# Optimization experiments

Measured on AMD Instinct MI355X. Metric: run time of the kernel, lower is better.

## Reference

```python
import jax, jax.numpy as jnp
import numpy as np

N_NODES = 50000
N_EDGES = 800000
IN_DIM = 128
HIDDEN = 128
OUT_DIM = 128


def setup_inputs() -> dict:
    key = jax.random.key(0)
    k1, k2, k3, k4, k5, k6 = jax.random.split(key, 6)
    X = jax.random.normal(k1, (N_NODES, IN_DIM), dtype=jnp.float32)
    W0 = jax.random.normal(k2, (HIDDEN, IN_DIM), dtype=jnp.float32) * (1.0 / np.sqrt(IN_DIM))
    W1 = jax.random.normal(k3, (OUT_DIM, HIDDEN), dtype=jnp.float32) * (1.0 / np.sqrt(HIDDEN))
    norm = jax.random.uniform(k4, (N_EDGES,), dtype=jnp.float32)
    src = jax.random.randint(k5, (N_EDGES,), 0, N_NODES, dtype=jnp.int32)
    dst = jax.random.randint(k6, (N_EDGES,), 0, N_NODES, dtype=jnp.int32)
    return {"X": X, "W0": W0, "W1": W1, "norm": norm, "src": src, "dst": dst}


def _propagate(S, src, dst, norm, n_nodes):
    # gather-scale-scatter: Z[dst] += S[src] * norm   (SpMM-style)
    msg = S[src] * norm[:, None]  # [E, d]
    return jax.ops.segment_sum(msg, dst, num_segments=n_nodes)


def reference(X, W0, W1, norm, src, dst):
    n = X.shape[0]
    # layer 1: linear (nn.Linear stores W as [out,in], so x @ W.T) + propagate + relu
    S0 = X @ W0.T                       # [N, hidden]
    H = jax.nn.relu(_propagate(S0, src, dst, norm, n))
    # dropout p=0.5 -> identity in eval mode (reference baseline)
    S1 = H @ W1.T                       # [N, out]
    Z = _propagate(S1, src, dst, norm, n)
    return (Z, H)
```

## Files before the change

### kernel.cpp

```cpp
#include <hip/hip_runtime.h>

#define DIM 128
#define NB 782
#define BCAP 1536

typedef __attribute__((ext_vector_type(8))) short bf16x8_t;
typedef __attribute__((ext_vector_type(4))) float f32x4_t;

__device__ __forceinline__ short f2bf(float f) {
    unsigned u = __float_as_uint(f);
    u += 0x7FFFu + ((u >> 16) & 1u);
    return (short)(u >> 16);
}
__device__ __forceinline__ float bf2f(short s) {
    return __uint_as_float(((unsigned)(unsigned short)s) << 16);
}

#define SC_VPT 16
__global__ __launch_bounds__(256) void bucket_scatter(const int* __restrict__ src,
                                                      const int* __restrict__ dst,
                                                      const float* __restrict__ norm,
                                                      int* __restrict__ bcursor,
                                                      int2* __restrict__ binned, int E) {
    __shared__ int hist[NB];
    __shared__ int base[NB];
    int t = threadIdx.x;
    for (int b = t; b < NB; b += 256) hist[b] = 0;
    __syncthreads();

    int e0 = blockIdx.x * (256 * SC_VPT);
    int bkts[SC_VPT];
    int pack[SC_VPT];
    int nrm[SC_VPT];
    #pragma unroll
    for (int k = 0; k < SC_VPT; k++) {
        int e = e0 + k * 256 + t;
        if (e < E) {
            int d = dst[e];
            bkts[k] = d >> 6;
            pack[k] = ((d & 63) << 26) | src[e];
            nrm[k]  = __float_as_int(norm[e]);
            atomicAdd(&hist[bkts[k]], 1);
        } else bkts[k] = -1;
    }
    __syncthreads();
    for (int b = t; b < NB; b += 256) {
        int c = hist[b];
        base[b] = b * BCAP + (c ? atomicAdd(&bcursor[b], c) : 0);
        hist[b] = 0;
    }
    __syncthreads();
    #pragma unroll
    for (int k = 0; k < SC_VPT; k++) {
        if (bkts[k] >= 0) {
            int pos = base[bkts[k]] + atomicAdd(&hist[bkts[k]], 1);
            binned[pos] = make_int2(pack[k], nrm[k]);
        }
    }
}


__global__ __launch_bounds__(256) void gemm_mfma(const float* __restrict__ A,
                                                 const float* __restrict__ W,
                                                 short* __restrict__ Cbf, int n,
                                                 int* __restrict__ bcursor_zero) {
    if (bcursor_zero != nullptr && blockIdx.x == 0) {
        for (int i = threadIdx.x; i < NB; i += 256) bcursor_zero[i] = 0;
    }

    int wave = threadIdx.x >> 6;
    int lane = threadIdx.x & 63;
    int l16  = lane & 15;
    int quad = lane >> 4;
    int r0 = blockIdx.x * 64 + wave * 16;

    int arow = r0 + l16;
    if (arow >= n) arow = n - 1;
    const float* Ar = A + (size_t)arow * DIM + quad * 8;

    bf16x8_t fa[4];
    #pragma unroll
    for (int kk = 0; kk < 4; kk++) {
        float4 x0 = *(const float4*)(Ar + kk * 32);
        float4 x1 = *(const float4*)(Ar + kk * 32 + 4);
        bf16x8_t f;
        f[0] = f2bf(x0.x); f[1] = f2bf(x0.y); f[2] = f2bf(x0.z); f[3] = f2bf(x0.w);
        f[4] = f2bf(x1.x); f[5] = f2bf(x1.y); f[6] = f2bf(x1.z); f[7] = f2bf(x1.w);
        fa[kk] = f;
    }

    #pragma unroll
    for (int ct = 0; ct < 8; ct++) {
        const float* Wr = W + (size_t)(ct * 16 + l16) * DIM + quad * 8;
        f32x4_t acc = {0.f, 0.f, 0.f, 0.f};
        #pragma unroll
        for (int kk = 0; kk < 4; kk++) {
            float4 w0 = *(const float4*)(Wr + kk * 32);
            float4 w1 = *(const float4*)(Wr + kk * 32 + 4);
            bf16x8_t fb;
            fb[0] = f2bf(w0.x); fb[1] = f2bf(w0.y); fb[2] = f2bf(w0.z); fb[3] = f2bf(w0.w);
            fb[4] = f2bf(w1.x); fb[5] = f2bf(w1.y); fb[6] = f2bf(w1.z); fb[7] = f2bf(w1.w);
            acc = __builtin_amdgcn_mfma_f32_16x16x32_bf16(fa[kk], fb, acc, 0, 0, 0);
        }
        #pragma unroll
        for (int j = 0; j < 4; j++) {
            int row = r0 + quad * 4 + j;
            if (row < n) Cbf[(size_t)row * DIM + ct * 16 + l16] = f2bf(acc[j]);
        }
    }
}


__global__ __launch_bounds__(512) void prop_bucket(const short* __restrict__ Sbf,
                                                   const int2* __restrict__ binned,
                                                   const int* __restrict__ bcnt,
                                                   float* __restrict__ out,
                                                   int n, int do_relu) {
    __shared__ int2 eds[BCAP];
    __shared__ int  hist[64];
    __shared__ int  offs_s[65];
    int b = blockIdx.x;
    int t = threadIdx.x;
    int cnt = bcnt[b];
    if (cnt > BCAP) cnt = BCAP;
    if (t < 64) hist[t] = 0;
    __syncthreads();

    const int2* eb = binned + (size_t)b * BCAP;
    for (int i = t; i < cnt; i += 512)
        atomicAdd(&hist[((unsigned)eb[i].x) >> 26], 1);
    __syncthreads();
    if (t < 64) {
        int v = hist[t];
        int s = v;
        #pragma unroll
        for (int o = 1; o < 64; o <<= 1) {
            int x = __shfl_up(s, o, 64);
            if (t >= o) s += x;
        }
        offs_s[t] = s - v;
        if (t == 63) offs_s[64] = s;
        hist[t] = s - v;
    }
    __syncthreads();
    for (int i = t; i < cnt; i += 512) {
        int2 e = eb[i];
        int pos = atomicAdd(&hist[((unsigned)e.x) >> 26], 1);
        eds[pos] = e;
    }
    __syncthreads();

    int wv   = t >> 6;
    int lane = t & 63;
    int q    = lane >> 4;
    int l16  = lane & 15;
    int node0 = b << 6;
    for (int nd = wv; nd < 64; nd += 8) {
        int beg = offs_s[nd];
        int end = offs_s[nd + 1];
        float acc[8] = {};
        int i = beg + q;
        for (; i + 4 < end; i += 8) {
            int2 e0 = eds[i];
            int2 e1 = eds[i + 4];
            bf16x8_t v0 = *(const bf16x8_t*)(Sbf + (size_t)((unsigned)e0.x & 0x3FFFFFF) * DIM + l16 * 8);
            bf16x8_t v1 = *(const bf16x8_t*)(Sbf + (size_t)((unsigned)e1.x & 0x3FFFFFF) * DIM + l16 * 8);
            float n0 = __int_as_float(e0.y);
            float n1 = __int_as_float(e1.y);
            #pragma unroll
            for (int j = 0; j < 8; j++) acc[j] += n0 * bf2f(v0[j]);
            #pragma unroll
            for (int j = 0; j < 8; j++) acc[j] += n1 * bf2f(v1[j]);
        }
        for (; i < end; i += 4) {
            int2 e = eds[i];
            bf16x8_t v = *(const bf16x8_t*)(Sbf + (size_t)((unsigned)e.x & 0x3FFFFFF) * DIM + l16 * 8);
            float nv = __int_as_float(e.y);
            #pragma unroll
            for (int j = 0; j < 8; j++) acc[j] += nv * bf2f(v[j]);
        }
        #pragma unroll
        for (int j = 0; j < 8; j++) {
            acc[j] += __shfl_xor(acc[j], 16, 64);
            acc[j] += __shfl_xor(acc[j], 32, 64);
        }
        int node = node0 + nd;
        if (q == 0 && node < n) {
            if (do_relu) {
                #pragma unroll
                for (int j = 0; j < 8; j++) acc[j] = fmaxf(acc[j], 0.f);
            }
            f32x4_t o0 = {acc[0], acc[1], acc[2], acc[3]};
            f32x4_t o1 = {acc[4], acc[5], acc[6], acc[7]};
            float* row = out + (size_t)node * DIM + l16 * 8;
            __builtin_nontemporal_store(o0, (f32x4_t*)row);
            __builtin_nontemporal_store(o1, (f32x4_t*)(row + 4));
        }
    }
}


extern "C" void kernel_launch(void* const* d_in, const int* in_sizes, int n_in,
                              void* d_out, int out_size, void* d_ws, size_t ws_size,
                              hipStream_t stream) {
    const float* X    = (const float*)d_in[0];
    const float* W0   = (const float*)d_in[1];
    const float* W1   = (const float*)d_in[2];
    const float* norm = (const float*)d_in[3];
    const int*   src  = (const int*)d_in[4];
    const int*   dst  = (const int*)d_in[5];

    const int N = in_sizes[0] / DIM;
    const int E = in_sizes[3];

    float* Z = (float*)d_out;
    float* H = (float*)d_out + (size_t)N * DIM;

    char* ws = (char*)d_ws;
    short* Sbf    = (short*)ws;
    size_t off    = (size_t)N * DIM * sizeof(short);
    int*   bcursor= (int*)(ws + off); off += (NB * 4 + 255) / 256 * 256;
    int2*  binned = (int2*)(ws + off); off += (size_t)NB * BCAP * 8;

    const int gemm_grid = (N + 63) / 64;

    gemm_mfma<<<gemm_grid, 256, 0, stream>>>(X, W0, Sbf, N, bcursor);
    bucket_scatter<<<(E + 256 * SC_VPT - 1) / (256 * SC_VPT), 256, 0, stream>>>(
        src, dst, norm, bcursor, binned, E);
    prop_bucket<<<NB, 512, 0, stream>>>(Sbf, binned, bcursor, H, N, 1);
    gemm_mfma<<<gemm_grid, 256, 0, stream>>>(H, W1, Sbf, N, nullptr);
    prop_bucket<<<NB, 512, 0, stream>>>(Sbf, binned, bcursor, Z, N, 0);
}
```

Before: 235.4 us.

## Fuse first GEMM with edge bucketing and reuse sorted edges in second propagate

Merges the first GEMM and the bucket-scatter kernel into a single launch, with blocks split by index, so the two independent phases can overlap. Zeroing of the bucket cursor moves to a hipMemsetAsync. The first propagate pass now writes its per-node sorted edge list and offsets to global memory. The second pass reads those back instead of re-histogramming and re-sorting in shared memory. This trades an extra global write and read of the edge list for removing the counting sort, and adds a memset launch.

```diff
diff --git a/kernel.cpp b/kernel.cpp
--- a/kernel.cpp
+++ b/kernel.cpp
@@ -3,6 +3,7 @@
 #define DIM 128
 #define NB 782
 #define BCAP 1536
+#define SC_VPT 16
 
 typedef __attribute__((ext_vector_type(8))) short bf16x8_t;
 typedef __attribute__((ext_vector_type(4))) float f32x4_t;
@@ -16,63 +17,14 @@
     return __uint_as_float(((unsigned)(unsigned short)s) << 16);
 }
 
-#define SC_VPT 16
-__global__ __launch_bounds__(256) void bucket_scatter(const int* __restrict__ src,
-                                                      const int* __restrict__ dst,
-                                                      const float* __restrict__ norm,
-                                                      int* __restrict__ bcursor,
-                                                      int2* __restrict__ binned, int E) {
-    __shared__ int hist[NB];
-    __shared__ int base[NB];
-    int t = threadIdx.x;
-    for (int b = t; b < NB; b += 256) hist[b] = 0;
-    __syncthreads();
-
-    int e0 = blockIdx.x * (256 * SC_VPT);
-    int bkts[SC_VPT];
-    int pack[SC_VPT];
-    int nrm[SC_VPT];
-    #pragma unroll
-    for (int k = 0; k < SC_VPT; k++) {
-        int e = e0 + k * 256 + t;
-        if (e < E) {
-            int d = dst[e];
-            bkts[k] = d >> 6;
-            pack[k] = ((d & 63) << 26) | src[e];
-            nrm[k]  = __float_as_int(norm[e]);
-            atomicAdd(&hist[bkts[k]], 1);
-        } else bkts[k] = -1;
-    }
-    __syncthreads();
-    for (int b = t; b < NB; b += 256) {
-        int c = hist[b];
-        base[b] = b * BCAP + (c ? atomicAdd(&bcursor[b], c) : 0);
-        hist[b] = 0;
-    }
-    __syncthreads();
-    #pragma unroll
-    for (int k = 0; k < SC_VPT; k++) {
-        if (bkts[k] >= 0) {
-            int pos = base[bkts[k]] + atomicAdd(&hist[bkts[k]], 1);
-            binned[pos] = make_int2(pack[k], nrm[k]);
-        }
-    }
-}
-
-
-__global__ __launch_bounds__(256) void gemm_mfma(const float* __restrict__ A,
-                                                 const float* __restrict__ W,
-                                                 short* __restrict__ Cbf, int n,
-                                                 int* __restrict__ bcursor_zero) {
-    if (bcursor_zero != nullptr && blockIdx.x == 0) {
-        for (int i = threadIdx.x; i < NB; i += 256) bcursor_zero[i] = 0;
-    }
-
+__device__ __forceinline__ void gemm_body(const float* __restrict__ A,
+                                          const float* __restrict__ W,
+                                          short* __restrict__ Cbf, int n, int blk) {
     int wave = threadIdx.x >> 6;
     int lane = threadIdx.x & 63;
     int l16  = lane & 15;
     int quad = lane >> 4;
-    int r0 = blockIdx.x * 64 + wave * 16;
+    int r0 = blk * 64 + wave * 16;
 
     int arow = r0 + l16;
     if (arow >= n) arow = n - 1;
@@ -110,74 +62,172 @@
     }
 }
 
+__device__ __forceinline__ void scatter_body(const int* __restrict__ src,
+                                             const int* __restrict__ dst,
+                                             const float* __restrict__ norm,
+                                             int* __restrict__ bcursor,
+                                             int2* __restrict__ binned, int E, int blk) {
+    __shared__ int hist[NB];
+    __shared__ int base[NB];
+    int t = threadIdx.x;
+    for (int b = t; b < NB; b += 256) hist[b] = 0;
+    __syncthreads();
+
+    int e0 = blk * (256 * SC_VPT);
+    int bkts[SC_VPT];
+    int pack[SC_VPT];
+    int nrm[SC_VPT];
+    #pragma unroll
+    for (int k = 0; k < SC_VPT; k++) {
+        int e = e0 + k * 256 + t;
+        if (e < E) {
+            int d = dst[e];
+            bkts[k] = d >> 6;
+            pack[k] = ((d & 63) << 26) | src[e];
+            nrm[k]  = __float_as_int(norm[e]);
+            atomicAdd(&hist[bkts[k]], 1);
+        } else bkts[k] = -1;
+    }
+    __syncthreads();
+    for (int b = t; b < NB; b += 256) {
+        int c = hist[b];
+        base[b] = b * BCAP + (c ? atomicAdd(&bcursor[b], c) : 0);
+        hist[b] = 0;
+    }
+    __syncthreads();
+    #pragma unroll
+    for (int k = 0; k < SC_VPT; k++) {
+        if (bkts[k] >= 0) {
+            int pos = base[bkts[k]] + atomicAdd(&hist[bkts[k]], 1);
+            binned[pos] = make_int2(pack[k], nrm[k]);
+        }
+    }
+}
+
+__global__ __launch_bounds__(256) void fused_gemm_scatter(
+        const float* __restrict__ X, const float* __restrict__ W0,
+        short* __restrict__ Sbf, int n,
+        const int* __restrict__ src, const int* __restrict__ dst,
+        const float* __restrict__ norm, int* __restrict__ bcursor,
+        int2* __restrict__ binned, int E, int gemmBlocks) {
+    if ((int)blockIdx.x < gemmBlocks)
+        gemm_body(X, W0, Sbf, n, blockIdx.x);
+    else
+        scatter_body(src, dst, norm, bcursor, binned, E, blockIdx.x - gemmBlocks);
+}
+
+__global__ __launch_bounds__(256) void gemm_mfma(const float* __restrict__ A,
+                                                 const float* __restrict__ W,
+                                                 short* __restrict__ Cbf, int n) {
+    gemm_body(A, W, Cbf, n, blockIdx.x);
+}
+
 
 __global__ __launch_bounds__(512) void prop_bucket(const short* __restrict__ Sbf,
                                                    const int2* __restrict__ binned,
                                                    const int* __restrict__ bcnt,
+                                                   int2* __restrict__ edges2,
+                                                   int* __restrict__ offs_g,
                                                    float* __restrict__ out,
-                                                   int n, int do_relu) {
+                                                   int n, int do_relu, int mode) {
+    __shared__ int2 raw[BCAP];
     __shared__ int2 eds[BCAP];
     __shared__ int  hist[64];
     __shared__ int  offs_s[65];
     int b = blockIdx.x;
     int t = threadIdx.x;
-    int cnt = bcnt[b];
-    if (cnt > BCAP) cnt = BCAP;
-    if (t < 64) hist[t] = 0;
-    __syncthreads();
-
-    const int2* eb = binned + (size_t)b * BCAP;
-    for (int i = t; i < cnt; i += 512)
-        atomicAdd(&hist[((unsigned)eb[i].x) >> 26], 1);
-    __syncthreads();
-    if (t < 64) {
-        int v = hist[t];
-        int s = v;
-        #pragma unroll
-        for (int o = 1; o < 64; o <<= 1) {
-            int x = __shfl_up(s, o, 64);
-            if (t >= o) s += x;
-        }
-        offs_s[t] = s - v;
-        if (t == 63) offs_s[64] = s;
-        hist[t] = s - v;
-    }
-    __syncthreads();
-    for (int i = t; i < cnt; i += 512) {
-        int2 e = eb[i];
-        int pos = atomicAdd(&hist[((unsigned)e.x) >> 26], 1);
-        eds[pos] = e;
-    }
-    __syncthreads();
+
+    if (mode == 0) {
+        int cnt = bcnt[b];
+        if (cnt > BCAP) cnt = BCAP;
+        if (t < 64) hist[t] = 0;
+        __syncthreads();
+        const int2* eb = binned + (size_t)b * BCAP;
+        for (int i = t; i < cnt; i += 512) {
+            int2 e = eb[i];
+            raw[i] = e;
+            atomicAdd(&hist[((unsigned)e.x) >> 26], 1);
+        }
+        __syncthreads();
+        if (t < 64) {
+            int v = hist[t];
+            int s = v;
+            #pragma unroll
+            for (int o = 1; o < 64; o <<= 1) {
+                int x = __shfl_up(s, o, 64);
+                if (t >= o) s += x;
+            }
+            offs_s[t] = s - v;
+            if (t == 63) offs_s[64] = s;
+            hist[t] = s - v;
+        }
+        __syncthreads();
+        for (int i = t; i < cnt; i += 512) {
+            int2 e = raw[i];
+            int pos = atomicAdd(&hist[((unsigned)e.x) >> 26], 1);
+            eds[pos] = e;
+        }
+        __syncthreads();
+        int2* e2 = edges2 + (size_t)b * BCAP;
+        for (int i = t; i < cnt; i += 512) e2[i] = eds[i];
+        if (t < 65) offs_g[b * 65 + t] = offs_s[t];
+    } else {
+        if (t < 65) offs_s[t] = offs_g[b * 65 + t];
+        __syncthreads();
+    }
 
     int wv   = t >> 6;
     int lane = t & 63;
     int q    = lane >> 4;
     int l16  = lane & 15;
     int node0 = b << 6;
+    const int2* eg = edges2 + (size_t)b * BCAP;
+
     for (int nd = wv; nd < 64; nd += 8) {
         int beg = offs_s[nd];
         int end = offs_s[nd + 1];
         float acc[8] = {};
         int i = beg + q;
-        for (; i + 4 < end; i += 8) {
-            int2 e0 = eds[i];
-            int2 e1 = eds[i + 4];
-            bf16x8_t v0 = *(const bf16x8_t*)(Sbf + (size_t)((unsigned)e0.x & 0x3FFFFFF) * DIM + l16 * 8);
-            bf16x8_t v1 = *(const bf16x8_t*)(Sbf + (size_t)((unsigned)e1.x & 0x3FFFFFF) * DIM + l16 * 8);
-            float n0 = __int_as_float(e0.y);
-            float n1 = __int_as_float(e1.y);
-            #pragma unroll
-            for (int j = 0; j < 8; j++) acc[j] += n0 * bf2f(v0[j]);
-            #pragma unroll
-            for (int j = 0; j < 8; j++) acc[j] += n1 * bf2f(v1[j]);
-        }
-        for (; i < end; i += 4) {
-            int2 e = eds[i];
-            bf16x8_t v = *(const bf16x8_t*)(Sbf + (size_t)((unsigned)e.x & 0x3FFFFFF) * DIM + l16 * 8);
-            float nv = __int_as_float(e.y);
-            #pragma unroll
-            for (int j = 0; j < 8; j++) acc[j] += nv * bf2f(v[j]);
+        if (mode == 0) {
+            for (; i + 4 < end; i += 8) {
+                int2 e0 = eds[i];
+                int2 e1 = eds[i + 4];
+                bf16x8_t v0 = *(const bf16x8_t*)(Sbf + (size_t)((unsigned)e0.x & 0x3FFFFFF) * DIM + l16 * 8);
+                bf16x8_t v1 = *(const bf16x8_t*)(Sbf + (size_t)((unsigned)e1.x & 0x3FFFFFF) * DIM + l16 * 8);
+                float n0 = __int_as_float(e0.y);
+                float n1 = __int_as_float(e1.y);
+                #pragma unroll
+                for (int j = 0; j < 8; j++) acc[j] += n0 * bf2f(v0[j]);
+                #pragma unroll
+                for (int j = 0; j < 8; j++) acc[j] += n1 * bf2f(v1[j]);
+            }
+            for (; i < end; i += 4) {
+                int2 e = eds[i];
+                bf16x8_t v = *(const bf16x8_t*)(Sbf + (size_t)((unsigned)e.x & 0x3FFFFFF) * DIM + l16 * 8);
+                float nv = __int_as_float(e.y);
+                #pragma unroll
+                for (int j = 0; j < 8; j++) acc[j] += nv * bf2f(v[j]);
+            }
+        } else {
+            for (; i + 4 < end; i += 8) {
+                int2 e0 = eg[i];
+                int2 e1 = eg[i + 4];
+                bf16x8_t v0 = *(const bf16x8_t*)(Sbf + (size_t)((unsigned)e0.x & 0x3FFFFFF) * DIM + l16 * 8);
+                bf16x8_t v1 = *(const bf16x8_t*)(Sbf + (size_t)((unsigned)e1.x & 0x3FFFFFF) * DIM + l16 * 8);
+                float n0 = __int_as_float(e0.y);
+                float n1 = __int_as_float(e1.y);
+                #pragma unroll
+                for (int j = 0; j < 8; j++) acc[j] += n0 * bf2f(v0[j]);
+                #pragma unroll
+                for (int j = 0; j < 8; j++) acc[j] += n1 * bf2f(v1[j]);
+            }
+            for (; i < end; i += 4) {
+                int2 e = eg[i];
+                bf16x8_t v = *(const bf16x8_t*)(Sbf + (size_t)((unsigned)e.x & 0x3FFFFFF) * DIM + l16 * 8);
+                float nv = __int_as_float(e.y);
+                #pragma unroll
+                for (int j = 0; j < 8; j++) acc[j] += nv * bf2f(v[j]);
+            }
         }
         #pragma unroll
         for (int j = 0; j < 8; j++) {
@@ -220,14 +270,17 @@
     short* Sbf    = (short*)ws;
     size_t off    = (size_t)N * DIM * sizeof(short);
     int*   bcursor= (int*)(ws + off); off += (NB * 4 + 255) / 256 * 256;
+    int*   offs_g = (int*)(ws + off); off += ((size_t)NB * 65 * 4 + 255) / 256 * 256;
     int2*  binned = (int2*)(ws + off); off += (size_t)NB * BCAP * 8;
-
-    const int gemm_grid = (N + 63) / 64;
-
-    gemm_mfma<<<gemm_grid, 256, 0, stream>>>(X, W0, Sbf, N, bcursor);
-    bucket_scatter<<<(E + 256 * SC_VPT - 1) / (256 * SC_VPT), 256, 0, stream>>>(
-        src, dst, norm, bcursor, binned, E);
-    prop_bucket<<<NB, 512, 0, stream>>>(Sbf, binned, bcursor, H, N, 1);
-    gemm_mfma<<<gemm_grid, 256, 0, stream>>>(H, W1, Sbf, N, nullptr);
-    prop_bucket<<<NB, 512, 0, stream>>>(Sbf, binned, bcursor, Z, N, 0);
-}
+    int2*  edges2 = (int2*)(ws + off); off += (size_t)NB * BCAP * 8;
+
+    const int gemmBlocks = (N + 63) / 64;
+    const int scBlocks   = (E + 256 * SC_VPT - 1) / (256 * SC_VPT);
+
+    hipMemsetAsync(bcursor, 0, NB * sizeof(int), stream);
+    fused_gemm_scatter<<<gemmBlocks + scBlocks, 256, 0, stream>>>(
+        X, W0, Sbf, N, src, dst, norm, bcursor, binned, E, gemmBlocks);
+    prop_bucket<<<NB, 512, 0, stream>>>(Sbf, binned, bcursor, edges2, offs_g, H, N, 1, 0);
+    gemm_mfma<<<gemmBlocks, 256, 0, stream>>>(H, W1, Sbf, N);
+    prop_bucket<<<NB, 512, 0, stream>>>(Sbf, binned, bcursor, edges2, offs_g, Z, N, 0, 1);
+}
```

Result: faster. 227.2 us (-3.5%).
